# Kernel optimization log

Hardware: AMD Instinct MI355X
Metric: run time of the kernel (lower is better)

## Reference

```python
import jax, jax.numpy as jnp
import numpy as np

HEADS = 8
MODEL_DIM = 64
IN_DIM = 512
FF_DIM = 2048
LN_EPS = 1e-5


def _ln(t, g, b):
    m = t.mean(-1, keepdims=True)
    v = ((t - m) ** 2).mean(-1, keepdims=True)
    return (t - m) * jax.lax.rsqrt(v + LN_EPS) * g + b


def setup_inputs() -> dict:
    key = jax.random.key(0)
    ks = jax.random.split(key, 12)
    s = 1.0 / np.sqrt(IN_DIM)
    x = jax.random.normal(ks[0], (8, 32, 32, IN_DIM), dtype=jnp.float32)
    Wq = jax.random.uniform(ks[1], (IN_DIM, HEADS * MODEL_DIM), jnp.float32, -s, s)
    Wk = jax.random.uniform(ks[2], (IN_DIM, HEADS * MODEL_DIM), jnp.float32, -s, s)
    Wv = jax.random.uniform(ks[3], (IN_DIM, HEADS * MODEL_DIM), jnp.float32, -s, s)
    Wo = jax.random.uniform(ks[4], (HEADS * MODEL_DIM, IN_DIM), jnp.float32, -s, s)
    ln1_g = jnp.ones((IN_DIM,), jnp.float32)
    ln1_b = jnp.zeros((IN_DIM,), jnp.float32)
    fc1_w = jax.random.uniform(ks[5], (IN_DIM, FF_DIM), jnp.float32, -s, s)
    fc1_b = jnp.zeros((FF_DIM,), jnp.float32)
    s2 = 1.0 / np.sqrt(FF_DIM)
    fc2_w = jax.random.uniform(ks[6], (FF_DIM, IN_DIM), jnp.float32, -s2, s2)
    fc2_b = jnp.zeros((IN_DIM,), jnp.float32)
    ln2_g = jnp.ones((IN_DIM,), jnp.float32)
    ln2_b = jnp.zeros((IN_DIM,), jnp.float32)
    return {"x": x, "Wq": Wq, "Wk": Wk, "Wv": Wv, "Wo": Wo,
            "ln1_g": ln1_g, "ln1_b": ln1_b,
            "fc1_w": fc1_w, "fc1_b": fc1_b, "fc2_w": fc2_w, "fc2_b": fc2_b,
            "ln2_g": ln2_g, "ln2_b": ln2_b}


def reference(x, Wq, Wk, Wv, Wo, ln1_g, ln1_b, fc1_w, fc1_b, fc2_w, fc2_b, ln2_g, ln2_b):
    bs, h, w, c = x.shape
    # --- BertSelfAttention (pre_norm=True) ---
    xn = _ln(x, ln1_g, ln1_b)
    Q = (xn @ Wq).reshape(bs, h, w, HEADS, MODEL_DIM)
    K = (xn @ Wk).reshape(bs, h, w, HEADS, MODEL_DIM)
    V = (xn @ Wv).reshape(bs, h, w, HEADS, MODEL_DIM)
    scores = jnp.einsum('bijhd,bklhd->bijhkl', Q, K) / jnp.sqrt(jnp.float32(MODEL_DIM))
    probs = jax.nn.softmax(scores.reshape(bs, h, w, HEADS, h * w), axis=-1)
    probs = probs.reshape(bs, h, w, HEADS, h, w)
    o = jnp.einsum('bijhkl,bklhd->bijhd', probs, V).reshape(bs, h, w, HEADS * MODEL_DIM)
    attn_out = o @ Wo + xn  # residual adds pre-normed x (as in the torch code)
    # --- Feedforward (pre_norm=True) ---
    yn = _ln(attn_out, ln2_g, ln2_b)
    out = jax.nn.relu(yn @ fc1_w + fc1_b) @ fc2_w + fc2_b + yn
    return (out, probs)
```

## Files before the change

### kernel.cpp

```cpp
#include <hip/hip_runtime.h>

typedef unsigned short u16;
typedef unsigned int   u32;
typedef short s16x8 __attribute__((ext_vector_type(8)));
typedef float f32x4 __attribute__((ext_vector_type(4)));

#define EPI_QK  0
#define EPI_VT  1
#define EPI_RES 2
#define EPI_FC1 3
#define EPI_FC2 4

__device__ __forceinline__ u16 f2bf(float f) {
    u32 u = __float_as_uint(f);
    u32 r = u + 0x7FFFu + ((u >> 16) & 1u);
    return (u16)(r >> 16);
}
__device__ __forceinline__ s16x8 ld8(const u16* p) {
    return *(const s16x8*)p;
}
__device__ __forceinline__ void gload_lds16(const void* g, void* l) {
    __builtin_amdgcn_global_load_lds(
        (const __attribute__((address_space(1))) unsigned int*)g,
        (__attribute__((address_space(3))) unsigned int*)l, 16, 0, 0);
}

__global__ __launch_bounds__(256) void transpose_bf16(
    const float* __restrict__ W, u16* __restrict__ Wt, int Kd, int Nd)
{
    __shared__ float tls[32][33];
    const int k0 = blockIdx.x * 32, n0 = blockIdx.y * 32;
    const int r = threadIdx.x >> 3, c4 = (threadIdx.x & 7) * 4;
    float4 v = *(const float4*)&W[(size_t)(k0 + r) * Nd + n0 + c4];
    tls[r][c4] = v.x; tls[r][c4 + 1] = v.y; tls[r][c4 + 2] = v.z; tls[r][c4 + 3] = v.w;
    __syncthreads();
    u32 lo = (u32)f2bf(tls[c4][r])     | ((u32)f2bf(tls[c4 + 1][r]) << 16);
    u32 hi = (u32)f2bf(tls[c4 + 2][r]) | ((u32)f2bf(tls[c4 + 3][r]) << 16);
    uint2 pk; pk.x = lo; pk.y = hi;
    *(uint2*)&Wt[(size_t)(n0 + r) * Kd + k0 + c4] = pk;
}

__global__ __launch_bounds__(256) void ln_kernel(
    const float* __restrict__ x, const float* __restrict__ g, const float* __restrict__ bb,
    float* __restrict__ of, u16* __restrict__ ob)
{
    const int wave = threadIdx.x >> 6, lane = threadIdx.x & 63;
    const int t = blockIdx.x * 4 + wave;
    const float* row = x + (size_t)t * 512;
    float4 v0 = *(const float4*)&row[lane * 8];
    float4 v1 = *(const float4*)&row[lane * 8 + 4];
    float s  = v0.x + v0.y + v0.z + v0.w + v1.x + v1.y + v1.z + v1.w;
    float sq = v0.x*v0.x + v0.y*v0.y + v0.z*v0.z + v0.w*v0.w
             + v1.x*v1.x + v1.y*v1.y + v1.z*v1.z + v1.w*v1.w;
#pragma unroll
    for (int o = 1; o < 64; o <<= 1) { s += __shfl_xor(s, o, 64); sq += __shfl_xor(sq, o, 64); }
    float mean = s * (1.f / 512.f);
    float var  = sq * (1.f / 512.f) - mean * mean;
    float rs = rsqrtf(var + 1e-5f);
    float4 g0 = *(const float4*)&g[lane * 8];
    float4 g1 = *(const float4*)&g[lane * 8 + 4];
    float4 b0 = *(const float4*)&bb[lane * 8];
    float4 b1 = *(const float4*)&bb[lane * 8 + 4];
    float y[8];
    y[0] = (v0.x - mean) * rs * g0.x + b0.x;
    y[1] = (v0.y - mean) * rs * g0.y + b0.y;
    y[2] = (v0.z - mean) * rs * g0.z + b0.z;
    y[3] = (v0.w - mean) * rs * g0.w + b0.w;
    y[4] = (v1.x - mean) * rs * g1.x + b1.x;
    y[5] = (v1.y - mean) * rs * g1.y + b1.y;
    y[6] = (v1.z - mean) * rs * g1.z + b1.z;
    y[7] = (v1.w - mean) * rs * g1.w + b1.w;
    float4 o0; o0.x = y[0]; o0.y = y[1]; o0.z = y[2]; o0.w = y[3];
    float4 o1; o1.x = y[4]; o1.y = y[5]; o1.z = y[6]; o1.w = y[7];
    *(float4*)&of[(size_t)t * 512 + lane * 8]     = o0;
    *(float4*)&of[(size_t)t * 512 + lane * 8 + 4] = o1;
    uint4 pb;
    pb.x = (u32)f2bf(y[0]) | ((u32)f2bf(y[1]) << 16);
    pb.y = (u32)f2bf(y[2]) | ((u32)f2bf(y[3]) << 16);
    pb.z = (u32)f2bf(y[4]) | ((u32)f2bf(y[5]) << 16);
    pb.w = (u32)f2bf(y[6]) | ((u32)f2bf(y[7]) << 16);
    *(uint4*)&ob[(size_t)t * 512 + lane * 8] = pb;
}

template<int EPI>
__global__ __launch_bounds__(256) void gemm128(
    const u16* __restrict__ A, const u16* __restrict__ Bt,
    void* __restrict__ Out, void* __restrict__ Out2,
    const float* __restrict__ bias, const float* __restrict__ res,
    int M, int N, int K)
{
    __shared__ u16 sA[128 * 32];
    __shared__ u16 sB[128 * 32];
    const int tid = threadIdx.x;
    const int wave = tid >> 6, lane = tid & 63;
    const int n0 = blockIdx.x * 128, m0 = blockIdx.y * 128;
    const int wr = (wave >> 1) * 64, wc = (wave & 1) * 64;
    const int lr = lane & 15, quad = lane >> 4;

    const int p0 = wave * 64 + lane;
    const int r0 = p0 >> 2,          c0 = p0 & 3;
    const int r1 = (p0 + 256) >> 2;
    const u16* gA0 = A  + (size_t)(m0 + r0) * K + c0 * 8;
    const u16* gA1 = A  + (size_t)(m0 + r1) * K + c0 * 8;
    const u16* gB0 = Bt + (size_t)(n0 + r0) * K + c0 * 8;
    const u16* gB1 = Bt + (size_t)(n0 + r1) * K + c0 * 8;
    u16* lA0 = sA + (size_t)(wave * 64) * 8;
    u16* lA1 = sA + (size_t)(256 + wave * 64) * 8;
    u16* lB0 = sB + (size_t)(wave * 64) * 8;
    u16* lB1 = sB + (size_t)(256 + wave * 64) * 8;

    f32x4 acc[4][4] = {};
    for (int k0 = 0; k0 < K; k0 += 32) {
        __syncthreads();
        gload_lds16(gA0 + k0, lA0);
        gload_lds16(gA1 + k0, lA1);
        gload_lds16(gB0 + k0, lB0);
        gload_lds16(gB1 + k0, lB1);
        __syncthreads();
        s16x8 a[4], b[4];
#pragma unroll
        for (int i = 0; i < 4; i++) a[i] = ld8(&sA[(wr + i * 16 + lr) * 32 + quad * 8]);
#pragma unroll
        for (int j = 0; j < 4; j++) b[j] = ld8(&sB[(wc + j * 16 + lr) * 32 + quad * 8]);
#pragma unroll
        for (int i = 0; i < 4; i++)
#pragma unroll
            for (int j = 0; j < 4; j++)
                acc[i][j] = __builtin_amdgcn_mfma_f32_16x16x32_bf16(a[i], b[j], acc[i][j], 0, 0, 0);
    }

#pragma unroll
    for (int i = 0; i < 4; i++)
#pragma unroll
    for (int j = 0; j < 4; j++)
#pragma unroll
    for (int r = 0; r < 4; r++) {
        int row = m0 + wr + i * 16 + quad * 4 + r;
        int col = n0 + wc + j * 16 + lr;
        float v = acc[i][j][r];
        if (EPI == EPI_QK) {
            u16* dst = (col < 512) ? (u16*)Out : (u16*)Out2;
            int c2 = col & 511;
            size_t idx = (size_t)((row >> 10) * 8 + (c2 >> 6)) * 65536
                       + (size_t)(row & 1023) * 64 + (c2 & 63);
            dst[idx] = f2bf(v);
        } else if (EPI == EPI_VT) {
            size_t idx = (size_t)((col >> 10) * 8 + (row >> 6)) * 65536
                       + (size_t)(row & 63) * 1024 + (col & 1023);
            ((u16*)Out)[idx] = f2bf(v);
        } else if (EPI == EPI_RES) {
            size_t idx = (size_t)row * N + col;
            ((float*)Out)[idx] = v + res[idx];
        } else if (EPI == EPI_FC1) {
            v += bias[col];
            v = fmaxf(v, 0.f);
            ((u16*)Out)[(size_t)row * N + col] = f2bf(v);
        } else {
            size_t idx = (size_t)row * N + col;
            ((float*)Out)[idx] = v + bias[col] + res[idx];
        }
    }
}

__global__ __launch_bounds__(256) void attn_kernel(
    const u16* __restrict__ Qs, const u16* __restrict__ Ks, const u16* __restrict__ Vts,
    float* __restrict__ probs, u16* __restrict__ Os)
{
    __shared__ u16 sQ[64 * 72];
    __shared__ u16 sK[64 * 72];
    __shared__ u16 sV[64 * 72];
    __shared__ u16 sP[4][16 * 72];
    const int bh = blockIdx.x;
    const int q0 = blockIdx.y * 64;
    const int b = bh >> 3, h = bh & 7;
    const int tid = threadIdx.x, wave = tid >> 6, lane = tid & 63;
    const int lr = lane & 15, quad = lane >> 4;
    const float scale = 0.125f;

    {
        const u16* qb = Qs + (size_t)bh * 65536 + (size_t)q0 * 64;
        for (int c = tid; c < 512; c += 256) {
            int r = c >> 3, off = (c & 7) * 8;
            *(uint4*)&sQ[r * 72 + off] = *(const uint4*)&qb[r * 64 + off];
        }
    }
    float l[4] = {0.f, 0.f, 0.f, 0.f};

    for (int kt = 0; kt < 16; ++kt) {
        __syncthreads();
        const u16* kb = Ks + (size_t)bh * 65536 + (size_t)kt * 4096;
        for (int c = tid; c < 512; c += 256) {
            int r = c >> 3, off = (c & 7) * 8;
            *(uint4*)&sK[r * 72 + off] = *(const uint4*)&kb[r * 64 + off];
        }
        __syncthreads();
        f32x4 s[4] = {};
#pragma unroll
        for (int ks = 0; ks < 2; ++ks) {
            s16x8 a = ld8(&sQ[(wave * 16 + lr) * 72 + ks * 32 + quad * 8]);
#pragma unroll
            for (int j = 0; j < 4; j++) {
                s16x8 bf = ld8(&sK[(j * 16 + lr) * 72 + ks * 32 + quad * 8]);
                s[j] = __builtin_amdgcn_mfma_f32_16x16x32_bf16(a, bf, s[j], 0, 0, 0);
            }
        }
#pragma unroll
        for (int j = 0; j < 4; j++)
#pragma unroll
            for (int r = 0; r < 4; r++) l[r] += __expf(s[j][r] * scale);
    }
#pragma unroll
    for (int r = 0; r < 4; r++) {
#pragma unroll
        for (int o = 1; o < 16; o <<= 1) l[r] += __shfl_xor(l[r], o, 64);
        l[r] = 1.f / l[r];
    }

    f32x4 o[4] = {};
    for (int kt = 0; kt < 16; ++kt) {
        __syncthreads();
        const u16* kb = Ks  + (size_t)bh * 65536 + (size_t)kt * 4096;
        const u16* vb = Vts + (size_t)bh * 65536 + (size_t)kt * 64;
        for (int c = tid; c < 512; c += 256) {
            int r = c >> 3, off = (c & 7) * 8;
            *(uint4*)&sK[r * 72 + off] = *(const uint4*)&kb[r * 64 + off];
            *(uint4*)&sV[r * 72 + off] = *(const uint4*)&vb[(size_t)r * 1024 + off];
        }
        __syncthreads();
        f32x4 s[4] = {};
#pragma unroll
        for (int ks = 0; ks < 2; ++ks) {
            s16x8 a = ld8(&sQ[(wave * 16 + lr) * 72 + ks * 32 + quad * 8]);
#pragma unroll
            for (int j = 0; j < 4; j++) {
                s16x8 bf = ld8(&sK[(j * 16 + lr) * 72 + ks * 32 + quad * 8]);
                s[j] = __builtin_amdgcn_mfma_f32_16x16x32_bf16(a, bf, s[j], 0, 0, 0);
            }
        }
#pragma unroll
        for (int j = 0; j < 4; j++) {
#pragma unroll
            for (int r = 0; r < 4; r++) {
                float p = __expf(s[j][r] * scale) * l[r];
                int q = q0 + wave * 16 + quad * 4 + r;
                probs[(size_t)(b * 1024 + q) * 8192 + h * 1024 + kt * 64 + j * 16 + lr] = p;
                sP[wave][(quad * 4 + r) * 72 + j * 16 + lr] = f2bf(p);
            }
        }
        asm volatile("s_waitcnt lgkmcnt(0)" ::: "memory");
#pragma unroll
        for (int ks = 0; ks < 2; ++ks) {
            s16x8 a = ld8(&sP[wave][lr * 72 + ks * 32 + quad * 8]);
#pragma unroll
            for (int jd = 0; jd < 4; jd++) {
                s16x8 bv = ld8(&sV[(jd * 16 + lr) * 72 + ks * 32 + quad * 8]);
                o[jd] = __builtin_amdgcn_mfma_f32_16x16x32_bf16(a, bv, o[jd], 0, 0, 0);
            }
        }
    }
#pragma unroll
    for (int jd = 0; jd < 4; jd++)
#pragma unroll
    for (int r = 0; r < 4; r++) {
        int q = q0 + wave * 16 + quad * 4 + r;
        int d = jd * 16 + lr;
        Os[(size_t)(b * 1024 + q) * 512 + h * 64 + d] = f2bf(o[jd][r]);
    }
}

extern "C" void kernel_launch(void* const* d_in, const int* in_sizes, int n_in,
                              void* d_out, int out_size, void* d_ws, size_t ws_size,
                              hipStream_t stream)
{
    const float* x     = (const float*)d_in[0];
    const float* Wq    = (const float*)d_in[1];
    const float* Wk    = (const float*)d_in[2];
    const float* Wv    = (const float*)d_in[3];
    const float* Wo    = (const float*)d_in[4];
    const float* ln1_g = (const float*)d_in[5];
    const float* ln1_b = (const float*)d_in[6];
    const float* fc1_w = (const float*)d_in[7];
    const float* fc1_b = (const float*)d_in[8];
    const float* fc2_w = (const float*)d_in[9];
    const float* fc2_b = (const float*)d_in[10];
    const float* ln2_g = (const float*)d_in[11];
    const float* ln2_b = (const float*)d_in[12];

    char* ws = (char*)d_ws;
    const size_t MB = 1024 * 1024;
    u16*   Q_s    = (u16*)(ws + 0);
    u16*   K_s    = (u16*)(ws + 8 * MB);
    u16*   Vt_s   = (u16*)(ws + 16 * MB);
    u16*   O_s    = (u16*)(ws + 24 * MB);
    u16*   hidden = (u16*)(ws + 0);
    float* xn_f   = (float*)(ws + 32 * MB);
    u16*   xn_b   = (u16*)(ws + 48 * MB);
    float* aout   = (float*)(ws + 56 * MB);
    float* yn_f   = (float*)(ws + 72 * MB);
    u16*   yn_b   = (u16*)(ws + 88 * MB);
    u16*   WqT  = (u16*)(ws + 96 * MB);
    u16*   WkT  = WqT + 512 * 512;
    u16*   WvT  = WkT + 512 * 512;
    u16*   WoT  = WvT + 512 * 512;
    u16*   fc1T = WoT + 512 * 512;
    u16*   fc2T = fc1T + 2048 * 512;

    float* out0  = (float*)d_out;
    float* probs = out0 + 4194304;

    dim3 blk(256);
    transpose_bf16<<<dim3(16, 16), blk, 0, stream>>>(Wq, WqT, 512, 512);
    transpose_bf16<<<dim3(16, 16), blk, 0, stream>>>(Wk, WkT, 512, 512);
    transpose_bf16<<<dim3(16, 16), blk, 0, stream>>>(Wv, WvT, 512, 512);
    transpose_bf16<<<dim3(16, 16), blk, 0, stream>>>(Wo, WoT, 512, 512);
    transpose_bf16<<<dim3(16, 64), blk, 0, stream>>>(fc1_w, fc1T, 512, 2048);
    transpose_bf16<<<dim3(64, 16), blk, 0, stream>>>(fc2_w, fc2T, 2048, 512);

    ln_kernel<<<2048, blk, 0, stream>>>(x, ln1_g, ln1_b, xn_f, xn_b);

    gemm128<EPI_QK><<<dim3(8, 64), blk, 0, stream>>>(
        xn_b, WqT, Q_s, K_s, nullptr, nullptr, 8192, 1024, 512);
    gemm128<EPI_VT><<<dim3(64, 4), blk, 0, stream>>>(
        WvT, xn_b, Vt_s, nullptr, nullptr, nullptr, 512, 8192, 512);

    attn_kernel<<<dim3(64, 16), blk, 0, stream>>>(Q_s, K_s, Vt_s, probs, O_s);

    gemm128<EPI_RES><<<dim3(4, 64), blk, 0, stream>>>(
        O_s, WoT, aout, nullptr, nullptr, xn_f, 8192, 512, 512);

    ln_kernel<<<2048, blk, 0, stream>>>(aout, ln2_g, ln2_b, yn_f, yn_b);

    gemm128<EPI_FC1><<<dim3(16, 64), blk, 0, stream>>>(
        yn_b, fc1T, hidden, nullptr, fc1_b, nullptr, 8192, 2048, 512);
    gemm128<EPI_FC2><<<dim3(4, 64), blk, 0, stream>>>(
        hidden, fc2T, out0, nullptr, fc2_b, yn_f, 8192, 512, 2048);
}
```

Before: 557.9 us.

## Double-buffer GEMM LDS tiles and load attention operands directly from global

The GEMM now keeps two shared-memory stages and prefetches the next K-tile with global_load_lds while the current tile feeds the MFMAs, cutting the loop to one barrier per iteration. The attention kernel no longer stages Q, K and V through shared memory. Each wave loads its MFMA operands straight from global memory into registers, which removes the block-wide barriers and LDS copies. In exchange, every wave issues redundant global loads of K and V and relies on the caches to absorb them. The GEMM also depends on the async LDS loads finishing before the barrier.

After: 646.2 us. 1.16x slower.

```diff
diff --git a/kernel.cpp b/kernel.cpp
--- a/kernel.cpp
+++ b/kernel.cpp
@@ -89,8 +89,8 @@
     const float* __restrict__ bias, const float* __restrict__ res,
     int M, int N, int K)
 {
-    __shared__ u16 sA[128 * 32];
-    __shared__ u16 sB[128 * 32];
+    __shared__ u16 sA[2][128 * 32];
+    __shared__ u16 sB[2][128 * 32];
     const int tid = threadIdx.x;
     const int wave = tid >> 6, lane = tid & 63;
     const int n0 = blockIdx.x * 128, m0 = blockIdx.y * 128;
@@ -104,29 +104,38 @@
     const u16* gA1 = A  + (size_t)(m0 + r1) * K + c0 * 8;
     const u16* gB0 = Bt + (size_t)(n0 + r0) * K + c0 * 8;
     const u16* gB1 = Bt + (size_t)(n0 + r1) * K + c0 * 8;
-    u16* lA0 = sA + (size_t)(wave * 64) * 8;
-    u16* lA1 = sA + (size_t)(256 + wave * 64) * 8;
-    u16* lB0 = sB + (size_t)(wave * 64) * 8;
-    u16* lB1 = sB + (size_t)(256 + wave * 64) * 8;
+    const int lo0 = (wave * 64) * 8;
+    const int lo1 = (256 + wave * 64) * 8;
 
     f32x4 acc[4][4] = {};
-    for (int k0 = 0; k0 < K; k0 += 32) {
+    const int nt = K >> 5;
+
+    gload_lds16(gA0, &sA[0][lo0]);
+    gload_lds16(gA1, &sA[0][lo1]);
+    gload_lds16(gB0, &sB[0][lo0]);
+    gload_lds16(gB1, &sB[0][lo1]);
+
+    int cur = 0;
+    for (int t = 0; t < nt; ++t) {
         __syncthreads();
-        gload_lds16(gA0 + k0, lA0);
-        gload_lds16(gA1 + k0, lA1);
-        gload_lds16(gB0 + k0, lB0);
-        gload_lds16(gB1 + k0, lB1);
-        __syncthreads();
+        if (t + 1 < nt) {
+            const int k0 = (t + 1) << 5;
+            gload_lds16(gA0 + k0, &sA[cur ^ 1][lo0]);
+            gload_lds16(gA1 + k0, &sA[cur ^ 1][lo1]);
+            gload_lds16(gB0 + k0, &sB[cur ^ 1][lo0]);
+            gload_lds16(gB1 + k0, &sB[cur ^ 1][lo1]);
+        }
         s16x8 a[4], b[4];
 #pragma unroll
-        for (int i = 0; i < 4; i++) a[i] = ld8(&sA[(wr + i * 16 + lr) * 32 + quad * 8]);
-#pragma unroll
-        for (int j = 0; j < 4; j++) b[j] = ld8(&sB[(wc + j * 16 + lr) * 32 + quad * 8]);
+        for (int i = 0; i < 4; i++) a[i] = ld8(&sA[cur][(wr + i * 16 + lr) * 32 + quad * 8]);
+#pragma unroll
+        for (int j = 0; j < 4; j++) b[j] = ld8(&sB[cur][(wc + j * 16 + lr) * 32 + quad * 8]);
 #pragma unroll
         for (int i = 0; i < 4; i++)
 #pragma unroll
             for (int j = 0; j < 4; j++)
                 acc[i][j] = __builtin_amdgcn_mfma_f32_16x16x32_bf16(a[i], b[j], acc[i][j], 0, 0, 0);
+        cur ^= 1;
     }
 
 #pragma unroll
@@ -166,9 +175,6 @@
     const u16* __restrict__ Qs, const u16* __restrict__ Ks, const u16* __restrict__ Vts,
     float* __restrict__ probs, u16* __restrict__ Os)
 {
-    __shared__ u16 sQ[64 * 72];
-    __shared__ u16 sK[64 * 72];
-    __shared__ u16 sV[64 * 72];
     __shared__ u16 sP[4][16 * 72];
     const int bh = blockIdx.x;
     const int q0 = blockIdx.y * 64;
@@ -177,32 +183,22 @@
     const int lr = lane & 15, quad = lane >> 4;
     const float scale = 0.125f;
 
-    {
-        const u16* qb = Qs + (size_t)bh * 65536 + (size_t)q0 * 64;
-        for (int c = tid; c < 512; c += 256) {
-            int r = c >> 3, off = (c & 7) * 8;
-            *(uint4*)&sQ[r * 72 + off] = *(const uint4*)&qb[r * 64 + off];
-        }
-    }
+    const u16* qb = Qs + (size_t)bh * 65536 + (size_t)(q0 + wave * 16 + lr) * 64 + quad * 8;
+    const s16x8 aq0 = ld8(qb);
+    const s16x8 aq1 = ld8(qb + 32);
+
+    const u16* kb = Ks  + (size_t)bh * 65536 + (size_t)lr * 64   + quad * 8;
+    const u16* vb = Vts + (size_t)bh * 65536 + (size_t)lr * 1024 + quad * 8;
+
     float l[4] = {0.f, 0.f, 0.f, 0.f};
 
     for (int kt = 0; kt < 16; ++kt) {
-        __syncthreads();
-        const u16* kb = Ks + (size_t)bh * 65536 + (size_t)kt * 4096;
-        for (int c = tid; c < 512; c += 256) {
-            int r = c >> 3, off = (c & 7) * 8;
-            *(uint4*)&sK[r * 72 + off] = *(const uint4*)&kb[r * 64 + off];
-        }
-        __syncthreads();
+        const u16* kk = kb + (size_t)kt * 4096;
         f32x4 s[4] = {};
 #pragma unroll
-        for (int ks = 0; ks < 2; ++ks) {
-            s16x8 a = ld8(&sQ[(wave * 16 + lr) * 72 + ks * 32 + quad * 8]);
-#pragma unroll
-            for (int j = 0; j < 4; j++) {
-                s16x8 bf = ld8(&sK[(j * 16 + lr) * 72 + ks * 32 + quad * 8]);
-                s[j] = __builtin_amdgcn_mfma_f32_16x16x32_bf16(a, bf, s[j], 0, 0, 0);
-            }
+        for (int j = 0; j < 4; j++) {
+            s[j] = __builtin_amdgcn_mfma_f32_16x16x32_bf16(aq0, ld8(kk + j * 1024),      s[j], 0, 0, 0);
+            s[j] = __builtin_amdgcn_mfma_f32_16x16x32_bf16(aq1, ld8(kk + j * 1024 + 32), s[j], 0, 0, 0);
         }
 #pragma unroll
         for (int j = 0; j < 4; j++)
@@ -218,24 +214,12 @@
 
     f32x4 o[4] = {};
     for (int kt = 0; kt < 16; ++kt) {
-        __syncthreads();
-        const u16* kb = Ks  + (size_t)bh * 65536 + (size_t)kt * 4096;
-        const u16* vb = Vts + (size_t)bh * 65536 + (size_t)kt * 64;
-        for (int c = tid; c < 512; c += 256) {
-            int r = c >> 3, off = (c & 7) * 8;
-            *(uint4*)&sK[r * 72 + off] = *(const uint4*)&kb[r * 64 + off];
-            *(uint4*)&sV[r * 72 + off] = *(const uint4*)&vb[(size_t)r * 1024 + off];
-        }
-        __syncthreads();
+        const u16* kk = kb + (size_t)kt * 4096;
         f32x4 s[4] = {};
 #pragma unroll
-        for (int ks = 0; ks < 2; ++ks) {
-            s16x8 a = ld8(&sQ[(wave * 16 + lr) * 72 + ks * 32 + quad * 8]);
-#pragma unroll
-            for (int j = 0; j < 4; j++) {
-                s16x8 bf = ld8(&sK[(j * 16 + lr) * 72 + ks * 32 + quad * 8]);
-                s[j] = __builtin_amdgcn_mfma_f32_16x16x32_bf16(a, bf, s[j], 0, 0, 0);
-            }
+        for (int j = 0; j < 4; j++) {
+            s[j] = __builtin_amdgcn_mfma_f32_16x16x32_bf16(aq0, ld8(kk + j * 1024),      s[j], 0, 0, 0);
+            s[j] = __builtin_amdgcn_mfma_f32_16x16x32_bf16(aq1, ld8(kk + j * 1024 + 32), s[j], 0, 0, 0);
         }
 #pragma unroll
         for (int j = 0; j < 4; j++) {
@@ -253,7 +237,7 @@
             s16x8 a = ld8(&sP[wave][lr * 72 + ks * 32 + quad * 8]);
 #pragma unroll
             for (int jd = 0; jd < 4; jd++) {
-                s16x8 bv = ld8(&sV[(jd * 16 + lr) * 72 + ks * 32 + quad * 8]);
+                s16x8 bv = ld8(vb + (size_t)jd * 16384 + kt * 64 + ks * 32);
                 o[jd] = __builtin_amdgcn_mfma_f32_16x16x32_bf16(a, bv, o[jd], 0, 0, 0);
             }
         }
```

## Double-buffer K/V tiles, keep Q in registers, vectorize probs stores in attention

Applied to the files above, without the earlier changes.

The attention kernel now double-buffers the K and V tiles in shared memory. Each iteration prefetches the next tile into registers during compute and writes it to the spare buffer afterwards, so each loop needs one barrier instead of two. Q fragments are held in registers instead of shared memory, and the MFMA operands are swapped so each lane holds four consecutive keys. That layout lets the probability output go out as 16-byte nontemporal stores and the bf16 probs go to shared memory as packed 8-byte writes, at the cost of more register pressure from the prefetch registers.

Measured after the change: 542.5 us. 2.8% less time.

```diff
diff --git a/kernel.cpp b/kernel.cpp
--- a/kernel.cpp
+++ b/kernel.cpp
@@ -166,9 +166,8 @@
     const u16* __restrict__ Qs, const u16* __restrict__ Ks, const u16* __restrict__ Vts,
     float* __restrict__ probs, u16* __restrict__ Os)
 {
-    __shared__ u16 sQ[64 * 72];
-    __shared__ u16 sK[64 * 72];
-    __shared__ u16 sV[64 * 72];
+    __shared__ u16 sK[2][64 * 72];
+    __shared__ u16 sV[2][64 * 72];
     __shared__ u16 sP[4][16 * 72];
     const int bh = blockIdx.x;
     const int q0 = blockIdx.y * 64;
@@ -177,75 +176,104 @@
     const int lr = lane & 15, quad = lane >> 4;
     const float scale = 0.125f;
 
+    const u16* qb = Qs + (size_t)bh * 65536 + (size_t)(q0 + wave * 16 + lr) * 64 + quad * 8;
+    const s16x8 bq0 = ld8(qb);
+    const s16x8 bq1 = ld8(qb + 32);
+
+    const int sr0 = tid >> 3, sr1 = sr0 + 32;
+    const int sc  = (tid & 7) * 8;
+    const u16* Kg = Ks  + (size_t)bh * 65536;
+    const u16* Vg = Vts + (size_t)bh * 65536;
+
     {
-        const u16* qb = Qs + (size_t)bh * 65536 + (size_t)q0 * 64;
-        for (int c = tid; c < 512; c += 256) {
-            int r = c >> 3, off = (c & 7) * 8;
-            *(uint4*)&sQ[r * 72 + off] = *(const uint4*)&qb[r * 64 + off];
-        }
-    }
-    float l[4] = {0.f, 0.f, 0.f, 0.f};
-
+        uint4 a0 = *(const uint4*)&Kg[(size_t)sr0 * 64 + sc];
+        uint4 a1 = *(const uint4*)&Kg[(size_t)sr1 * 64 + sc];
+        *(uint4*)&sK[0][sr0 * 72 + sc] = a0;
+        *(uint4*)&sK[0][sr1 * 72 + sc] = a1;
+    }
+    float lsum = 0.f;
+    int cur = 0;
     for (int kt = 0; kt < 16; ++kt) {
         __syncthreads();
-        const u16* kb = Ks + (size_t)bh * 65536 + (size_t)kt * 4096;
-        for (int c = tid; c < 512; c += 256) {
-            int r = c >> 3, off = (c & 7) * 8;
-            *(uint4*)&sK[r * 72 + off] = *(const uint4*)&kb[r * 64 + off];
-        }
-        __syncthreads();
+        uint4 pk0, pk1;
+        const bool pf = (kt + 1 < 16);
+        if (pf) {
+            const u16* kn = Kg + (size_t)(kt + 1) * 4096;
+            pk0 = *(const uint4*)&kn[(size_t)sr0 * 64 + sc];
+            pk1 = *(const uint4*)&kn[(size_t)sr1 * 64 + sc];
+        }
         f32x4 s[4] = {};
 #pragma unroll
         for (int ks = 0; ks < 2; ++ks) {
-            s16x8 a = ld8(&sQ[(wave * 16 + lr) * 72 + ks * 32 + quad * 8]);
+            const s16x8 bq = ks ? bq1 : bq0;
 #pragma unroll
             for (int j = 0; j < 4; j++) {
-                s16x8 bf = ld8(&sK[(j * 16 + lr) * 72 + ks * 32 + quad * 8]);
-                s[j] = __builtin_amdgcn_mfma_f32_16x16x32_bf16(a, bf, s[j], 0, 0, 0);
+                s16x8 ak = ld8(&sK[cur][(j * 16 + lr) * 72 + ks * 32 + quad * 8]);
+                s[j] = __builtin_amdgcn_mfma_f32_16x16x32_bf16(ak, bq, s[j], 0, 0, 0);
             }
         }
 #pragma unroll
         for (int j = 0; j < 4; j++)
 #pragma unroll
-            for (int r = 0; r < 4; r++) l[r] += __expf(s[j][r] * scale);
-    }
-#pragma unroll
-    for (int r = 0; r < 4; r++) {
-#pragma unroll
-        for (int o = 1; o < 16; o <<= 1) l[r] += __shfl_xor(l[r], o, 64);
-        l[r] = 1.f / l[r];
-    }
-
+            for (int r = 0; r < 4; r++) lsum += __expf(s[j][r] * scale);
+        if (pf) {
+            *(uint4*)&sK[cur ^ 1][sr0 * 72 + sc] = pk0;
+            *(uint4*)&sK[cur ^ 1][sr1 * 72 + sc] = pk1;
+        }
+        cur ^= 1;
+    }
+    lsum += __shfl_xor(lsum, 16, 64);
+    lsum += __shfl_xor(lsum, 32, 64);
+    const float linv = 1.f / lsum;
+
+    {
+        uint4 a0 = *(const uint4*)&Kg[(size_t)sr0 * 64 + sc];
+        uint4 a1 = *(const uint4*)&Kg[(size_t)sr1 * 64 + sc];
+        uint4 b0 = *(const uint4*)&Vg[(size_t)sr0 * 1024 + sc];
+        uint4 b1 = *(const uint4*)&Vg[(size_t)sr1 * 1024 + sc];
+        *(uint4*)&sK[0][sr0 * 72 + sc] = a0;
+        *(uint4*)&sK[0][sr1 * 72 + sc] = a1;
+        *(uint4*)&sV[0][sr0 * 72 + sc] = b0;
+        *(uint4*)&sV[0][sr1 * 72 + sc] = b1;
+    }
+    float* pbase = probs + ((size_t)(b * 1024 + q0 + wave * 16 + lr)) * 8192
+                 + h * 1024 + quad * 4;
     f32x4 o[4] = {};
+    cur = 0;
     for (int kt = 0; kt < 16; ++kt) {
         __syncthreads();
-        const u16* kb = Ks  + (size_t)bh * 65536 + (size_t)kt * 4096;
-        const u16* vb = Vts + (size_t)bh * 65536 + (size_t)kt * 64;
-        for (int c = tid; c < 512; c += 256) {
-            int r = c >> 3, off = (c & 7) * 8;
-            *(uint4*)&sK[r * 72 + off] = *(const uint4*)&kb[r * 64 + off];
-            *(uint4*)&sV[r * 72 + off] = *(const uint4*)&vb[(size_t)r * 1024 + off];
-        }
-        __syncthreads();
+        uint4 pk0, pk1, pv0, pv1;
+        const bool pf = (kt + 1 < 16);
+        if (pf) {
+            const u16* kn = Kg + (size_t)(kt + 1) * 4096;
+            const u16* vn = Vg + (size_t)(kt + 1) * 64;
+            pk0 = *(const uint4*)&kn[(size_t)sr0 * 64 + sc];
+            pk1 = *(const uint4*)&kn[(size_t)sr1 * 64 + sc];
+            pv0 = *(const uint4*)&vn[(size_t)sr0 * 1024 + sc];
+            pv1 = *(const uint4*)&vn[(size_t)sr1 * 1024 + sc];
+        }
         f32x4 s[4] = {};
 #pragma unroll
         for (int ks = 0; ks < 2; ++ks) {
-            s16x8 a = ld8(&sQ[(wave * 16 + lr) * 72 + ks * 32 + quad * 8]);
+            const s16x8 bq = ks ? bq1 : bq0;
 #pragma unroll
             for (int j = 0; j < 4; j++) {
-                s16x8 bf = ld8(&sK[(j * 16 + lr) * 72 + ks * 32 + quad * 8]);
-                s[j] = __builtin_amdgcn_mfma_f32_16x16x32_bf16(a, bf, s[j], 0, 0, 0);
+                s16x8 ak = ld8(&sK[cur][(j * 16 + lr) * 72 + ks * 32 + quad * 8]);
+                s[j] = __builtin_amdgcn_mfma_f32_16x16x32_bf16(ak, bq, s[j], 0, 0, 0);
             }
         }
 #pragma unroll
         for (int j = 0; j < 4; j++) {
-#pragma unroll
-            for (int r = 0; r < 4; r++) {
-                float p = __expf(s[j][r] * scale) * l[r];
-                int q = q0 + wave * 16 + quad * 4 + r;
-                probs[(size_t)(b * 1024 + q) * 8192 + h * 1024 + kt * 64 + j * 16 + lr] = p;
-                sP[wave][(quad * 4 + r) * 72 + j * 16 + lr] = f2bf(p);
-            }
+            float p0 = __expf(s[j][0] * scale) * linv;
+            float p1 = __expf(s[j][1] * scale) * linv;
+            float p2 = __expf(s[j][2] * scale) * linv;
+            float p3 = __expf(s[j][3] * scale) * linv;
+            f32x4 pq; pq[0] = p0; pq[1] = p1; pq[2] = p2; pq[3] = p3;
+            __builtin_nontemporal_store(pq, (f32x4*)&pbase[kt * 64 + j * 16]);
+            uint2 pb2;
+            pb2.x = (u32)f2bf(p0) | ((u32)f2bf(p1) << 16);
+            pb2.y = (u32)f2bf(p2) | ((u32)f2bf(p3) << 16);
+            *(uint2*)&sP[wave][lr * 72 + j * 16 + quad * 4] = pb2;
         }
         asm volatile("s_waitcnt lgkmcnt(0)" ::: "memory");
 #pragma unroll
@@ -253,10 +281,17 @@
             s16x8 a = ld8(&sP[wave][lr * 72 + ks * 32 + quad * 8]);
 #pragma unroll
             for (int jd = 0; jd < 4; jd++) {
-                s16x8 bv = ld8(&sV[(jd * 16 + lr) * 72 + ks * 32 + quad * 8]);
+                s16x8 bv = ld8(&sV[cur][(jd * 16 + lr) * 72 + ks * 32 + quad * 8]);
                 o[jd] = __builtin_amdgcn_mfma_f32_16x16x32_bf16(a, bv, o[jd], 0, 0, 0);
             }
         }
+        if (pf) {
+            *(uint4*)&sK[cur ^ 1][sr0 * 72 + sc] = pk0;
+            *(uint4*)&sK[cur ^ 1][sr1 * 72 + sc] = pk1;
+            *(uint4*)&sV[cur ^ 1][sr0 * 72 + sc] = pv0;
+            *(uint4*)&sV[cur ^ 1][sr1 * 72 + sc] = pv1;
+        }
+        cur ^= 1;
     }
 #pragma unroll
     for (int jd = 0; jd < 4; jd++)
```
